# Kernel tuning notes

Measured on AMD Instinct MI355X. Metric: run time of the kernel, lower is better.

The kernel has to match this reference:

```python
import jax, jax.numpy as jnp
import numpy as np

D_MODEL = 1024
NHEAD = 16
HEAD_DIM = D_MODEL // NHEAD
HIDDEN = 4 * D_MODEL  # SwiGLU hidden_dim
B, L = 2, 2048
EPS = 1e-8


def _alibi_slopes(n):
    # standard ALiBi slopes: geometric sequence 2^(-8/n * i)
    return np.array([2 ** (-8.0 / n * (i + 1)) for i in range(n)], dtype=np.float32)


def setup_inputs() -> dict:
    key = jax.random.key(0)
    ks = jax.random.split(key, 10)
    x = jax.random.normal(ks[0], (B, L, D_MODEL), dtype=jnp.float32)
    # causal mask: True where attention is disallowed (j > i)
    attn_mask = jnp.triu(jnp.ones((L, L), dtype=bool), k=1)[None, None]
    # ALiBi bias: -slope * (i - j) for j <= i; value on masked positions irrelevant
    pos = jnp.arange(L)
    dist = (pos[:, None] - pos[None, :]).astype(jnp.float32)  # [L,L]
    slopes = jnp.asarray(_alibi_slopes(NHEAD))
    alibi_bias = (-slopes[:, None, None] * dist)[None]  # [1,H,L,L]
    s = 0.02
    w_qkv = jax.random.normal(ks[1], (D_MODEL, 3 * D_MODEL), dtype=jnp.float32) * s
    b_qkv = jnp.zeros((3 * D_MODEL,), jnp.float32)
    w_o = jax.random.normal(ks[2], (D_MODEL, D_MODEL), dtype=jnp.float32) * s
    b_o = jnp.zeros((D_MODEL,), jnp.float32)
    scale1 = jnp.ones((D_MODEL,), jnp.float32)
    scale2 = jnp.ones((D_MODEL,), jnp.float32)
    w1 = jax.random.normal(ks[3], (D_MODEL, 2 * HIDDEN), dtype=jnp.float32) * s
    b1 = jnp.zeros((2 * HIDDEN,), jnp.float32)
    w2 = jax.random.normal(ks[4], (HIDDEN, D_MODEL), dtype=jnp.float32) * s
    b2 = jnp.zeros((D_MODEL,), jnp.float32)
    return dict(x=x, attn_mask=attn_mask, alibi_bias=alibi_bias,
                w_qkv=w_qkv, b_qkv=b_qkv, w_o=w_o, b_o=b_o,
                scale1=scale1, scale2=scale2, w1=w1, b1=b1, w2=w2, b2=b2)


def rmsnorm(x, scale):
    return scale * (x * jax.lax.rsqrt(jnp.mean(x * x, axis=-1, keepdims=True) + EPS))


def reference(x, attn_mask, alibi_bias, w_qkv, b_qkv, w_o, b_o,
              scale1, scale2, w1, b1, w2, b2):
    Bv, Lv, D = x.shape
    xn = rmsnorm(x, scale1)
    qkv = xn @ w_qkv + b_qkv  # [B,L,3D]
    q, k, v = jnp.split(qkv, 3, axis=-1)
    def to_heads(t):
        return t.reshape(Bv, Lv, NHEAD, HEAD_DIM).transpose(0, 2, 1, 3)  # [B,H,L,Dh]
    q, k, v = to_heads(q), to_heads(k), to_heads(v)
    scores = jnp.einsum('bhqd,bhkd->bhqk', q, k) / (HEAD_DIM ** 0.5)
    scores = scores + alibi_bias[:, :, :Lv, :Lv]
    scores = jnp.where(attn_mask, -jnp.inf, scores)
    attn = jax.nn.softmax(scores, axis=-1)
    out = jnp.einsum('bhqk,bhkd->bhqd', attn, v)  # [B,H,L,Dh]
    out = out.transpose(0, 2, 1, 3).reshape(Bv, Lv, D)
    x = x + (out @ w_o + b_o)
    # SwiGLU FFN
    h = rmsnorm(x, scale2) @ w1 + b1
    x_proj, gate = jnp.split(h, 2, axis=-1)
    ffn = (jax.nn.silu(gate) * x_proj) @ w2 + b2
    return x + ffn
```

## Files before the change

### kernel.cpp

```cpp
#include <hip/hip_runtime.h>
#include <hip/hip_bf16.h>
#include <stdint.h>

typedef __hip_bfloat16 bf16;
typedef __bf16 bf16x8 __attribute__((ext_vector_type(8)));
typedef float f32x4 __attribute__((ext_vector_type(4)));

#define DM   1024
#define LSEQ 2048
#define NH   16
#define DH   64
#define BB   2
#define HID  4096
#define MROWS (BB*LSEQ)
#define QLD  (3*DM)

__device__ __forceinline__ void load_lds16(const void* g, void* l) {
    __builtin_amdgcn_global_load_lds(
        (const __attribute__((address_space(1))) unsigned int*)g,
        (__attribute__((address_space(3))) unsigned int*)l, 16, 0, 0);
}

__global__ __launch_bounds__(256)
void transpose_all(const float* __restrict__ wqkv, const float* __restrict__ wo,
                   const float* __restrict__ w1, const float* __restrict__ w2,
                   bf16* __restrict__ wqkvT, bf16* __restrict__ woT,
                   bf16* __restrict__ w1T, bf16* __restrict__ w2T) {
    int bid = blockIdx.x;
    const float* src; bf16* dst; int R, C, bx, by; bool inter = false;
    if (bid < 3072)       { src = wqkv; dst = wqkvT; R = 1024; C = 3072; bx = bid % 96;  by = bid / 96; }
    else if (bid < 4096)  { bid -= 3072;  src = wo; dst = woT;  R = 1024; C = 1024; bx = bid % 32;  by = bid / 32; }
    else if (bid < 12288) { bid -= 4096;  src = w1; dst = w1T;  R = 1024; C = 8192; bx = bid % 256; by = bid / 256; inter = true; }
    else                  { bid -= 12288; src = w2; dst = w2T;  R = 4096; C = 1024; bx = bid % 32;  by = bid / 32; }
    __shared__ float tile[32][33];
    const int c0 = bx * 32, r0 = by * 32;
    const int tx = threadIdx.x & 31, ty = threadIdx.x >> 5;
#pragma unroll
    for (int i = 0; i < 32; i += 8)
        tile[ty + i][tx] = src[(size_t)(r0 + ty + i) * C + c0 + tx];
    __syncthreads();
#pragma unroll
    for (int i = 0; i < 32; i += 8) {
        const int c = c0 + ty + i;
        const int drow = inter ? ((c < HID) ? 2 * c : 2 * (c - HID) + 1) : c;
        dst[(size_t)drow * R + r0 + tx] = __float2bfloat16(tile[tx][ty + i]);
    }
}

__global__ __launch_bounds__(256)
void v_transpose(const bf16* __restrict__ qkv, bf16* __restrict__ vt) {
    const int bh = blockIdx.z, b = bh >> 4, h = bh & 15;
    const int l0 = blockIdx.x * 32, d0 = blockIdx.y * 32;
    __shared__ bf16 tile[32][33];
    const int tx = threadIdx.x & 31, ty = threadIdx.x >> 5;
#pragma unroll
    for (int i = 0; i < 32; i += 8)
        tile[ty + i][tx] = qkv[((size_t)b * LSEQ + l0 + ty + i) * QLD + 2 * DM + h * DH + d0 + tx];
    __syncthreads();
#pragma unroll
    for (int i = 0; i < 32; i += 8)
        vt[((size_t)bh * DH + d0 + ty + i) * LSEQ + l0 + tx] = tile[tx][ty + i];
}

__global__ __launch_bounds__(256)
void rmsnorm_cast(const float* __restrict__ x, const float* __restrict__ scale,
                  bf16* __restrict__ out) {
    const int row = blockIdx.x;
    const int tid = threadIdx.x;
    const float4 v = ((const float4*)(x + (size_t)row * DM))[tid];
    float ss = v.x * v.x + v.y * v.y + v.z * v.z + v.w * v.w;
#pragma unroll
    for (int off = 32; off >= 1; off >>= 1) ss += __shfl_xor(ss, off);
    __shared__ float part[4];
    if ((tid & 63) == 0) part[tid >> 6] = ss;
    __syncthreads();
    const float tot = part[0] + part[1] + part[2] + part[3];
    const float rs = rsqrtf(tot * (1.0f / DM) + 1e-8f);
    const float4 s = ((const float4*)scale)[tid];
    union { bf16 h[4]; uint2 u; } pk;
    pk.h[0] = __float2bfloat16(v.x * rs * s.x);
    pk.h[1] = __float2bfloat16(v.y * rs * s.y);
    pk.h[2] = __float2bfloat16(v.z * rs * s.z);
    pk.h[3] = __float2bfloat16(v.w * rs * s.w);
    ((uint2*)(out + (size_t)row * DM))[tid] = pk.u;
}

template <int KDIM, int NN, typename Epi>
__global__ __launch_bounds__(256, 2)
void gemm_bt(const bf16* __restrict__ A, const bf16* __restrict__ Bt, Epi epi) {
    __shared__ __align__(16) bf16 sA[128 * 32];
    __shared__ __align__(16) bf16 sB[128 * 32];
    constexpr int NPX = NN / 8;
    const int bid = blockIdx.x;
    const int xcd = bid & 7, loc = bid >> 3;
    const int nb = xcd * NPX + (loc % NPX), mb = loc / NPX;
    const int m0 = mb * 128, n0 = nb * 128;
    const int tid = threadIdx.x;
    const int wave = tid >> 6, lane = tid & 63;
    const int lo = lane & 15, hi = lane >> 4;
    const int wm = wave & 1, wn = wave >> 1;
    const int rowA = lane >> 2, cc = (lane & 3) * 8;

    f32x4 acc[4][4];
#pragma unroll
    for (int i = 0; i < 4; i++)
#pragma unroll
        for (int j = 0; j < 4; j++) acc[i][j] = (f32x4){0.f, 0.f, 0.f, 0.f};

    constexpr int NK = KDIM / 32;
    for (int kt = 0; kt < NK; ++kt) {
        const int k0 = kt * 32;
#pragma unroll
        for (int i = 0; i < 2; ++i) {
            const int slot = wave * 2 + i;
            load_lds16(A + (size_t)(m0 + slot * 16 + rowA) * KDIM + k0 + cc, &sA[slot * 512]);
            load_lds16(Bt + (size_t)(n0 + slot * 16 + rowA) * KDIM + k0 + cc, &sB[slot * 512]);
        }
        __syncthreads();
        bf16x8 a[4], b[4];
#pragma unroll
        for (int i = 0; i < 4; i++)
            a[i] = *(const bf16x8*)&sA[(wm * 64 + i * 16 + lo) * 32 + hi * 8];
#pragma unroll
        for (int j = 0; j < 4; j++)
            b[j] = *(const bf16x8*)&sB[(wn * 64 + j * 16 + lo) * 32 + hi * 8];
#pragma unroll
        for (int i = 0; i < 4; i++)
#pragma unroll
            for (int j = 0; j < 4; j++)
                acc[i][j] = __builtin_amdgcn_mfma_f32_16x16x32_bf16(a[i], b[j], acc[i][j], 0, 0, 0);
        __syncthreads();
    }
#pragma unroll
    for (int i = 0; i < 4; i++) {
        const int row = m0 + wm * 64 + i * 16 + hi * 4;
#pragma unroll
        for (int j = 0; j < 4; j++) {
            const int col = n0 + wn * 64 + j * 16 + lo;
#pragma unroll
            for (int r = 0; r < 4; r++) epi(row + r, col, acc[i][j][r]);
        }
    }
}

struct EpiBiasBF16 {
    const float* bias; bf16* out; int ldc;
    __device__ void operator()(int row, int col, float val) const {
        out[(size_t)row * ldc + col] = __float2bfloat16(val + bias[col]);
    }
};
struct EpiBiasResidF32 {
    const float* bias; const float* res; float* out; int ldc;
    __device__ void operator()(int row, int col, float val) const {
        const size_t idx = (size_t)row * ldc + col;
        out[idx] = val + bias[col] + res[idx];
    }
};
struct EpiSwiGLU {
    const float* b1; bf16* out;
    __device__ void operator()(int row, int col, float val) const {
        const int orig = (col >> 1) + ((col & 1) ? HID : 0);
        const float v = val + b1[orig];
        const float other = __shfl_xor(v, 1);
        const float g = other;
        const float s = g / (1.f + __expf(-g));
        if (!(threadIdx.x & 1))
            out[(size_t)row * HID + (col >> 1)] = __float2bfloat16(s * v);
    }
};

__global__ __launch_bounds__(256, 2)
void attn_flash(const bf16* __restrict__ qkv, const bf16* __restrict__ Vt,
                bf16* __restrict__ O) {
    const int bh = blockIdx.x;
    const int qt = gridDim.y - 1 - blockIdx.y;
    const int b = bh >> 4, h = bh & 15;
    const int tid = threadIdx.x, wave = tid >> 6, lane = tid & 63;
    const int lo = lane & 15, hi = lane >> 4;
    __shared__ __align__(16) bf16 sQ[64 * 64];
    __shared__ __align__(16) bf16 sK[64 * 64];
    __shared__ __align__(16) bf16 sV[64 * 64];
    __shared__ __align__(16) bf16 sP[4][16 * 64];

    const float LOG2E = 1.44269504088896340736f;
    const float slope2 = exp2f(-0.5f * (float)(h + 1)) * LOG2E;
    const float qscale = 0.125f * LOG2E;
    const float SHIFT = 34.0f;
    const int q0 = qt * 64;
    const bf16* Qb = qkv + (size_t)b * LSEQ * QLD + h * DH;
    const bf16* Kb = Qb + DM;
    const bf16* Vb = Vt + (size_t)bh * DH * LSEQ;

#pragma unroll
    for (int i = 0; i < 2; ++i) {
        const int s = wave * 2 + i;
        load_lds16(Qb + (size_t)(q0 + s * 8 + (lane >> 3)) * QLD + (lane & 7) * 8, &sQ[s * 512]);
    }
    __syncthreads();
    bf16x8 aq0 = *(const bf16x8*)&sQ[(wave * 16 + lo) * 64 + hi * 8];
    bf16x8 aq1 = *(const bf16x8*)&sQ[(wave * 16 + lo) * 64 + 32 + hi * 8];

    bf16x8 vone;
#pragma unroll
    for (int t = 0; t < 8; t++) vone[t] = (__bf16)1.0f;

    f32x4 accO[4];
#pragma unroll
    for (int j = 0; j < 4; j++) accO[j] = (f32x4){0.f, 0.f, 0.f, 0.f};
    f32x4 accL = (f32x4){0.f, 0.f, 0.f, 0.f};
    const int irow0 = q0 + wave * 16 + hi * 4;

    for (int kt = 0; kt <= qt; ++kt) {
        __syncthreads();
#pragma unroll
        for (int i = 0; i < 2; ++i) {
            const int s = wave * 2 + i;
            load_lds16(Kb + (size_t)(kt * 64 + s * 8 + (lane >> 3)) * QLD + (lane & 7) * 8, &sK[s * 512]);
            load_lds16(Vb + (size_t)(s * 8 + (lane >> 3)) * LSEQ + kt * 64 + (lane & 7) * 8, &sV[s * 512]);
        }
        __syncthreads();

#pragma unroll
        for (int j = 0; j < 4; j++) {
            bf16x8 bk0 = *(const bf16x8*)&sK[(j * 16 + lo) * 64 + hi * 8];
            bf16x8 bk1 = *(const bf16x8*)&sK[(j * 16 + lo) * 64 + 32 + hi * 8];
            f32x4 z = (f32x4){0.f, 0.f, 0.f, 0.f};
            z = __builtin_amdgcn_mfma_f32_16x16x32_bf16(aq0, bk0, z, 0, 0, 0);
            z = __builtin_amdgcn_mfma_f32_16x16x32_bf16(aq1, bk1, z, 0, 0, 0);
            const int jg = kt * 64 + j * 16 + lo;
#pragma unroll
            for (int r = 0; r < 4; r++) {
                const int ig = irow0 + r;
                const float pv = (jg > ig) ? 0.f
                    : exp2f(z[r] * qscale - slope2 * (float)(ig - jg) - SHIFT);
                sP[wave][(hi * 4 + r) * 64 + j * 16 + lo] = __float2bfloat16(pv);
            }
        }
        bf16x8 ap0 = *(const bf16x8*)&sP[wave][lo * 64 + hi * 8];
        bf16x8 ap1 = *(const bf16x8*)&sP[wave][lo * 64 + 32 + hi * 8];
        accL = __builtin_amdgcn_mfma_f32_16x16x32_bf16(ap0, vone, accL, 0, 0, 0);
        accL = __builtin_amdgcn_mfma_f32_16x16x32_bf16(ap1, vone, accL, 0, 0, 0);
#pragma unroll
        for (int j = 0; j < 4; j++) {
            bf16x8 bv0 = *(const bf16x8*)&sV[(j * 16 + lo) * 64 + hi * 8];
            bf16x8 bv1 = *(const bf16x8*)&sV[(j * 16 + lo) * 64 + 32 + hi * 8];
            accO[j] = __builtin_amdgcn_mfma_f32_16x16x32_bf16(ap0, bv0, accO[j], 0, 0, 0);
            accO[j] = __builtin_amdgcn_mfma_f32_16x16x32_bf16(ap1, bv1, accO[j], 0, 0, 0);
        }
    }
    bf16* Ob = O + (size_t)b * LSEQ * DM + (size_t)h * DH;
#pragma unroll
    for (int r = 0; r < 4; r++) {
        const float inv = 1.0f / accL[r];
        const int row = q0 + wave * 16 + hi * 4 + r;
#pragma unroll
        for (int j = 0; j < 4; j++)
            Ob[(size_t)row * DM + j * 16 + lo] = __float2bfloat16(accO[j][r] * inv);
    }
}

extern "C" void kernel_launch(void* const* d_in, const int* in_sizes, int n_in,
                              void* d_out, int out_size, void* d_ws, size_t ws_size,
                              hipStream_t stream) {
    const float* x      = (const float*)d_in[0];
    const float* w_qkv  = (const float*)d_in[3];
    const float* b_qkv  = (const float*)d_in[4];
    const float* w_o    = (const float*)d_in[5];
    const float* b_o    = (const float*)d_in[6];
    const float* scale1 = (const float*)d_in[7];
    const float* scale2 = (const float*)d_in[8];
    const float* w1     = (const float*)d_in[9];
    const float* b1     = (const float*)d_in[10];
    const float* w2     = (const float*)d_in[11];
    const float* b2     = (const float*)d_in[12];
    float* out = (float*)d_out;

    uint8_t* w = (uint8_t*)d_ws;
    size_t off = 0;
    auto take = [&](size_t bytes) { void* p = w + off; off += (bytes + 255) & ~(size_t)255; return p; };
    bf16* xn    = (bf16*)take((size_t)MROWS * DM * 2);
    bf16* wqkvT = (bf16*)take((size_t)3 * DM * DM * 2);
    bf16* woT   = (bf16*)take((size_t)DM * DM * 2);
    bf16* w1T   = (bf16*)take((size_t)2 * HID * DM * 2);
    bf16* w2T   = (bf16*)take((size_t)DM * HID * 2);
    bf16* qkvb  = (bf16*)take((size_t)MROWS * QLD * 2);
    bf16* vt    = (bf16*)take((size_t)MROWS * DM * 2);
    bf16* ao    = (bf16*)take((size_t)MROWS * DM * 2);
    float* x1   = (float*)take((size_t)MROWS * DM * 4);
    bf16* xn2   = (bf16*)take((size_t)MROWS * DM * 2);
    bf16* ffn   = (bf16*)take((size_t)MROWS * HID * 2);

    transpose_all<<<16384, 256, 0, stream>>>(w_qkv, w_o, w1, w2, wqkvT, woT, w1T, w2T);
    rmsnorm_cast<<<MROWS, 256, 0, stream>>>(x, scale1, xn);

    EpiBiasBF16 e1{b_qkv, qkvb, QLD};
    gemm_bt<DM, 24, EpiBiasBF16><<<32 * 24, 256, 0, stream>>>(xn, wqkvT, e1);

    v_transpose<<<dim3(LSEQ / 32, DH / 32, BB * NH), 256, 0, stream>>>(qkvb, vt);
    attn_flash<<<dim3(BB * NH, LSEQ / 64), 256, 0, stream>>>(qkvb, vt, ao);

    EpiBiasResidF32 e2{b_o, x, x1, DM};
    gemm_bt<DM, 8, EpiBiasResidF32><<<32 * 8, 256, 0, stream>>>(ao, woT, e2);

    rmsnorm_cast<<<MROWS, 256, 0, stream>>>(x1, scale2, xn2);

    EpiSwiGLU e3{b1, ffn};
    gemm_bt<DM, 64, EpiSwiGLU><<<32 * 64, 256, 0, stream>>>(xn2, w1T, e3);

    EpiBiasResidF32 e4{b2, x1, out, DM};
    gemm_bt<HID, 8, EpiBiasResidF32><<<32 * 8, 256, 0, stream>>>(ffn, w2T, e4);
}
```

Before: 703.4 us.

## Triple-buffer LDS tiles in GEMM and attention to overlap loads with MFMA

Both the GEMM and flash-attention kernels now use three LDS buffers. The next K-tile is prefetched with global_load_lds before computing on the current one, using s_waitcnt vmcnt(4) and a raw s_barrier in place of two __syncthreads per iteration. The goal is to hide global-memory latency behind matrix-core work and halve the barrier count. It also raises the GEMM launch-bounds occupancy hint to 3 blocks per CU, at the cost of more LDS per block and more register pressure. Ordering relies on the prefetch into the buffer used two iterations earlier being safe after the single barrier.

```diff
diff --git a/kernel.cpp b/kernel.cpp
--- a/kernel.cpp
+++ b/kernel.cpp
@@ -86,10 +86,10 @@
 }
 
 template <int KDIM, int NN, typename Epi>
-__global__ __launch_bounds__(256, 2)
+__global__ __launch_bounds__(256, 3)
 void gemm_bt(const bf16* __restrict__ A, const bf16* __restrict__ Bt, Epi epi) {
-    __shared__ __align__(16) bf16 sA[128 * 32];
-    __shared__ __align__(16) bf16 sB[128 * 32];
+    __shared__ __align__(16) bf16 sA[3][128 * 32];
+    __shared__ __align__(16) bf16 sB[3][128 * 32];
     constexpr int NPX = NN / 8;
     const int bid = blockIdx.x;
     const int xcd = bid & 7, loc = bid >> 3;
@@ -100,6 +100,20 @@
     const int lo = lane & 15, hi = lane >> 4;
     const int wm = wave & 1, wn = wave >> 1;
     const int rowA = lane >> 2, cc = (lane & 3) * 8;
+    const int slot0 = wave * 2, slot1 = wave * 2 + 1;
+
+    const bf16* Ag0 = A + (size_t)(m0 + slot0 * 16 + rowA) * KDIM + cc;
+    const bf16* Ag1 = A + (size_t)(m0 + slot1 * 16 + rowA) * KDIM + cc;
+    const bf16* Bg0 = Bt + (size_t)(n0 + slot0 * 16 + rowA) * KDIM + cc;
+    const bf16* Bg1 = Bt + (size_t)(n0 + slot1 * 16 + rowA) * KDIM + cc;
+
+    auto stage = [&](int kt, int buf) {
+        const int k0 = kt * 32;
+        load_lds16(Ag0 + k0, &sA[buf][slot0 * 512]);
+        load_lds16(Ag1 + k0, &sA[buf][slot1 * 512]);
+        load_lds16(Bg0 + k0, &sB[buf][slot0 * 512]);
+        load_lds16(Bg1 + k0, &sB[buf][slot1 * 512]);
+    };
 
     f32x4 acc[4][4];
 #pragma unroll
@@ -108,28 +122,32 @@
         for (int j = 0; j < 4; j++) acc[i][j] = (f32x4){0.f, 0.f, 0.f, 0.f};
 
     constexpr int NK = KDIM / 32;
+    stage(0, 0);
+    int bc = 0;
     for (int kt = 0; kt < NK; ++kt) {
-        const int k0 = kt * 32;
-#pragma unroll
-        for (int i = 0; i < 2; ++i) {
-            const int slot = wave * 2 + i;
-            load_lds16(A + (size_t)(m0 + slot * 16 + rowA) * KDIM + k0 + cc, &sA[slot * 512]);
-            load_lds16(Bt + (size_t)(n0 + slot * 16 + rowA) * KDIM + k0 + cc, &sB[slot * 512]);
-        }
-        __syncthreads();
+        const int bn = (bc == 2) ? 0 : bc + 1;
+        if (kt + 1 < NK) {
+            stage(kt + 1, bn);
+            asm volatile("s_waitcnt vmcnt(4)" ::: "memory");
+        } else {
+            asm volatile("s_waitcnt vmcnt(0)" ::: "memory");
+        }
+        asm volatile("s_barrier" ::: "memory");
+        const bf16* cA = sA[bc];
+        const bf16* cB = sB[bc];
         bf16x8 a[4], b[4];
 #pragma unroll
         for (int i = 0; i < 4; i++)
-            a[i] = *(const bf16x8*)&sA[(wm * 64 + i * 16 + lo) * 32 + hi * 8];
+            a[i] = *(const bf16x8*)&cA[(wm * 64 + i * 16 + lo) * 32 + hi * 8];
 #pragma unroll
         for (int j = 0; j < 4; j++)
-            b[j] = *(const bf16x8*)&sB[(wn * 64 + j * 16 + lo) * 32 + hi * 8];
+            b[j] = *(const bf16x8*)&cB[(wn * 64 + j * 16 + lo) * 32 + hi * 8];
 #pragma unroll
         for (int i = 0; i < 4; i++)
 #pragma unroll
             for (int j = 0; j < 4; j++)
                 acc[i][j] = __builtin_amdgcn_mfma_f32_16x16x32_bf16(a[i], b[j], acc[i][j], 0, 0, 0);
-        __syncthreads();
+        bc = bn;
     }
 #pragma unroll
     for (int i = 0; i < 4; i++) {
@@ -178,8 +196,8 @@
     const int tid = threadIdx.x, wave = tid >> 6, lane = tid & 63;
     const int lo = lane & 15, hi = lane >> 4;
     __shared__ __align__(16) bf16 sQ[64 * 64];
-    __shared__ __align__(16) bf16 sK[64 * 64];
-    __shared__ __align__(16) bf16 sV[64 * 64];
+    __shared__ __align__(16) bf16 sK[3][64 * 64];
+    __shared__ __align__(16) bf16 sV[3][64 * 64];
     __shared__ __align__(16) bf16 sP[4][16 * 64];
 
     const float LOG2E = 1.44269504088896340736f;
@@ -191,6 +209,14 @@
     const bf16* Kb = Qb + DM;
     const bf16* Vb = Vt + (size_t)bh * DH * LSEQ;
 
+    const int s0 = wave * 2, s1 = wave * 2 + 1;
+    auto stageKV = [&](int kt, int buf) {
+        load_lds16(Kb + (size_t)(kt * 64 + s0 * 8 + (lane >> 3)) * QLD + (lane & 7) * 8, &sK[buf][s0 * 512]);
+        load_lds16(Kb + (size_t)(kt * 64 + s1 * 8 + (lane >> 3)) * QLD + (lane & 7) * 8, &sK[buf][s1 * 512]);
+        load_lds16(Vb + (size_t)(s0 * 8 + (lane >> 3)) * LSEQ + kt * 64 + (lane & 7) * 8, &sV[buf][s0 * 512]);
+        load_lds16(Vb + (size_t)(s1 * 8 + (lane >> 3)) * LSEQ + kt * 64 + (lane & 7) * 8, &sV[buf][s1 * 512]);
+    };
+
 #pragma unroll
     for (int i = 0; i < 2; ++i) {
         const int s = wave * 2 + i;
@@ -210,20 +236,22 @@
     f32x4 accL = (f32x4){0.f, 0.f, 0.f, 0.f};
     const int irow0 = q0 + wave * 16 + hi * 4;
 
+    stageKV(0, 0);
+    int bc = 0;
     for (int kt = 0; kt <= qt; ++kt) {
-        __syncthreads();
-#pragma unroll
-        for (int i = 0; i < 2; ++i) {
-            const int s = wave * 2 + i;
-            load_lds16(Kb + (size_t)(kt * 64 + s * 8 + (lane >> 3)) * QLD + (lane & 7) * 8, &sK[s * 512]);
-            load_lds16(Vb + (size_t)(s * 8 + (lane >> 3)) * LSEQ + kt * 64 + (lane & 7) * 8, &sV[s * 512]);
-        }
-        __syncthreads();
+        const int bn = (bc == 2) ? 0 : bc + 1;
+        if (kt < qt) {
+            stageKV(kt + 1, bn);
+            asm volatile("s_waitcnt vmcnt(4)" ::: "memory");
+        } else {
+            asm volatile("s_waitcnt vmcnt(0)" ::: "memory");
+        }
+        asm volatile("s_barrier" ::: "memory");
 
 #pragma unroll
         for (int j = 0; j < 4; j++) {
-            bf16x8 bk0 = *(const bf16x8*)&sK[(j * 16 + lo) * 64 + hi * 8];
-            bf16x8 bk1 = *(const bf16x8*)&sK[(j * 16 + lo) * 64 + 32 + hi * 8];
+            bf16x8 bk0 = *(const bf16x8*)&sK[bc][(j * 16 + lo) * 64 + hi * 8];
+            bf16x8 bk1 = *(const bf16x8*)&sK[bc][(j * 16 + lo) * 64 + 32 + hi * 8];
             f32x4 z = (f32x4){0.f, 0.f, 0.f, 0.f};
             z = __builtin_amdgcn_mfma_f32_16x16x32_bf16(aq0, bk0, z, 0, 0, 0);
             z = __builtin_amdgcn_mfma_f32_16x16x32_bf16(aq1, bk1, z, 0, 0, 0);
@@ -242,11 +270,12 @@
         accL = __builtin_amdgcn_mfma_f32_16x16x32_bf16(ap1, vone, accL, 0, 0, 0);
 #pragma unroll
         for (int j = 0; j < 4; j++) {
-            bf16x8 bv0 = *(const bf16x8*)&sV[(j * 16 + lo) * 64 + hi * 8];
-            bf16x8 bv1 = *(const bf16x8*)&sV[(j * 16 + lo) * 64 + 32 + hi * 8];
+            bf16x8 bv0 = *(const bf16x8*)&sV[bc][(j * 16 + lo) * 64 + hi * 8];
+            bf16x8 bv1 = *(const bf16x8*)&sV[bc][(j * 16 + lo) * 64 + 32 + hi * 8];
             accO[j] = __builtin_amdgcn_mfma_f32_16x16x32_bf16(ap0, bv0, accO[j], 0, 0, 0);
             accO[j] = __builtin_amdgcn_mfma_f32_16x16x32_bf16(ap1, bv1, accO[j], 0, 0, 0);
         }
+        bc = bn;
     }
     bf16* Ob = O + (size_t)b * LSEQ * DM + (size_t)h * DH;
 #pragma unroll
```

After: 698.4 us. About the same (-0.7%).
